# Performance work log

Hardware: AMD Instinct MI355X
Metric: run time of the kernel (lower is better)

Reference implementation:

```python
import jax, jax.numpy as jnp
from jax import lax
import numpy as np

GAMMA = 1.0
BIG = 1e10  # stands in for +inf; exp(-BIG/gamma) == 0 in fp32, safe under autodiff


def cosine_distance_matrix(x, y):
    # x: [B,N,d], y: [B,M,d] -> D: [B,N,M] = 1 - cos(x_i, y_j)
    xn = x / (jnp.linalg.norm(x, axis=-1, keepdims=True) + 1e-8)
    yn = y / (jnp.linalg.norm(y, axis=-1, keepdims=True) + 1e-8)
    return 1.0 - jnp.einsum('bnd,bmd->bnm', xn, yn)


def soft_dtw(D, gamma):
    # D: [B,N,M]. Returns R[:, N, M] of the soft-DTW DP:
    # R[i,j] = D[i-1,j-1] + softmin(R[i-1,j-1], R[i-1,j], R[i,j-1])
    B, N, M = D.shape
    # column j=0: R[:,0,0]=0, R[:,i,0]=inf for i>=1  -> shape [B, N+1]
    init_col = jnp.concatenate([jnp.zeros((B, 1), D.dtype),
                                jnp.full((B, N), BIG, D.dtype)], axis=1)

    def col_step(prev_col, d_col):
        # prev_col: R[:, 0:N+1, j-1]  [B, N+1];  d_col: D[:, :, j-1]  [B, N]
        def row_step(carry, inp):
            r_diag, r_up, d = inp  # each [B]: R[i-1,j-1], R[i-1,j]... (see below)
            stacked = jnp.stack([r_diag, carry, r_up], axis=0)  # [3,B]
            softmin = -gamma * jax.nn.logsumexp(-stacked / gamma, axis=0)
            r = d + softmin
            return r, r
        # per-row inputs along i=1..N: diag=prev_col[i-1], up-in-column=prev_col[i]
        inputs = (prev_col[:, :-1].T, prev_col[:, 1:].T, d_col.T)  # each [N,B]
        _, rows = lax.scan(row_step, jnp.full((B,), BIG, D.dtype), inputs)
        new_col = jnp.concatenate([jnp.full((B, 1), BIG, D.dtype), rows.T], axis=1)
        return new_col, None

    final_col, _ = lax.scan(col_step, init_col, jnp.transpose(D, (2, 0, 1)))
    return final_col[:, -1]  # R[:, N, M]


def setup_inputs() -> dict:
    key = jax.random.key(0)
    k1, k2 = jax.random.split(key)
    B, N, M, d = 16, 1024, 1024, 128
    x = jax.random.normal(k1, (B, N, d), dtype=jnp.float32)
    y = jax.random.normal(k2, (B, M, d), dtype=jnp.float32)
    return {"x": x, "y": y}


def reference(x, y):
    D = cosine_distance_matrix(x, y)
    return soft_dtw(D, GAMMA)  # [B]
```

## Files before the change

### kernel.cpp

```cpp
#include <hip/hip_runtime.h>
#include <hip/hip_fp16.h>

#define BATCH 16
#define NROW 1024
#define MCOL 1024
#define DFEAT 128

#define R_DP 16
#define C_DP 8
#define NCH (MCOL / C_DP)
#define PSTRIDE 194

#define L2E 1.4426950408889634f
#define LN2 0.6931471805599453f

typedef __attribute__((ext_vector_type(8))) short short8;
typedef __attribute__((ext_vector_type(4))) float f32x4;

__device__ inline unsigned short f2bf(float f) {
  unsigned u = __float_as_uint(f);
  return (unsigned short)((u + 0x7fff + ((u >> 16) & 1)) >> 16);
}

__global__ __launch_bounds__(256) void norm_kernel(
    const float* __restrict__ x, const float* __restrict__ y,
    unsigned short* __restrict__ xnb, unsigned short* __restrict__ ynb) {
  int row = blockIdx.x * 4 + (threadIdx.x >> 6);
  int lane = threadIdx.x & 63;
  const float* src;
  unsigned short* dst;
  if (row < BATCH * NROW) {
    src = x + (size_t)row * DFEAT;
    dst = xnb + (size_t)row * DFEAT;
  } else {
    int r2 = row - BATCH * NROW;
    src = y + (size_t)r2 * DFEAT;
    dst = ynb + (size_t)r2 * DFEAT;
  }
  float2 v = *(const float2*)(src + lane * 2);
  float s = v.x * v.x + v.y * v.y;
  #pragma unroll
  for (int o = 32; o > 0; o >>= 1) s += __shfl_xor(s, o, 64);
  float inv = 1.0f / (sqrtf(s) + 1e-8f);
  unsigned short b0 = f2bf(v.x * inv), b1 = f2bf(v.y * inv);
  *(unsigned*)(dst + lane * 2) = (unsigned)b0 | ((unsigned)b1 << 16);
}

__global__ __launch_bounds__(256) void dist_kernel(
    const unsigned short* __restrict__ xnb, const unsigned short* __restrict__ ynb,
    __half* __restrict__ Dphase) {
  __shared__ __align__(16) unsigned char xsb[128 * 256];
  __shared__ __align__(16) unsigned char ysb[128 * 256];

  int b = blockIdx.z, ti0 = blockIdx.y, tj0 = blockIdx.x;
  int I0 = ti0 * 128, J0 = tj0 * 128;
  int tid = threadIdx.x;

  const uint4* xsrc = (const uint4*)(xnb + (size_t)(b * NROW + I0) * DFEAT);
  const uint4* ysrc = (const uint4*)(ynb + (size_t)(b * MCOL + J0) * DFEAT);
  #pragma unroll
  for (int it = 0; it < 8; ++it) {
    int idx = tid + it * 256;
    int row = idx >> 4, cb = (idx & 15) * 16;
    int swz = row * 256 + (cb ^ ((row & 7) << 4));
    *(uint4*)&xsb[swz] = xsrc[idx];
    *(uint4*)&ysb[swz] = ysrc[idx];
  }
  __syncthreads();

  int wid = tid >> 6, lane = tid & 63;
  int wi = wid >> 1, wj = wid & 1;
  int lr = lane & 15, lk = lane >> 4;

  f32x4 acc[4][4] = {};
  #pragma unroll
  for (int ks = 0; ks < 4; ++ks) {
    int cb = ks * 64 + lk * 16;
    short8 af[4], bf[4];
    #pragma unroll
    for (int ti = 0; ti < 4; ++ti) {
      int row = wi * 64 + ti * 16 + lr;
      af[ti] = *(short8*)&xsb[row * 256 + (cb ^ ((row & 7) << 4))];
    }
    #pragma unroll
    for (int tj = 0; tj < 4; ++tj) {
      int row = wj * 64 + tj * 16 + lr;
      bf[tj] = *(short8*)&ysb[row * 256 + (cb ^ ((row & 7) << 4))];
    }
    #pragma unroll
    for (int ti = 0; ti < 4; ++ti)
      #pragma unroll
      for (int tj = 0; tj < 4; ++tj)
        acc[ti][tj] = __builtin_amdgcn_mfma_f32_16x16x32_bf16(
            af[ti], bf[tj], acc[ti][tj], 0, 0, 0);
  }

  #pragma unroll
  for (int ti = 0; ti < 4; ++ti) {
    int gi0 = I0 + wi * 64 + ti * 16;
    int l = gi0 >> 4;
    #pragma unroll
    for (int tj = 0; tj < 4; ++tj) {
      int gj = J0 + wj * 64 + tj * 16 + lr;
      int c = gj >> 3, k = gj & 7;
      int p = c + l;
      #pragma unroll
      for (int v = 0; v < 4; ++v) {
        int r = lk * 4 + v;
        float d = 1.0f - acc[ti][tj][v];
        size_t off = ((((size_t)b * PSTRIDE + p) * R_DP + r) * 64 + l) * C_DP + k;
        Dphase[off] = __float2half(exp2f(-d * L2E));
      }
    }
  }
}

__device__ __forceinline__ float shup(float x, bool edge) {
  int xi = __float_as_int(x);
  int sh = __builtin_amdgcn_update_dpp(xi, xi, 0x111, 0xF, 0xF, false);
  int bc = __builtin_amdgcn_update_dpp(xi, xi, 0x142, 0xF, 0xF, false);
  return __int_as_float(edge ? bc : sh);
}

#define MIXMUL_LO(A, h, s) \
  asm("v_fma_mix_f32 %0, %1, %2, %3 op_sel_hi:[1,0,0]" : "=v"(A) : "v"(h), "v"(s), "v"(fzero))
#define MIXMUL_HI(A, h, s) \
  asm("v_fma_mix_f32 %0, %1, %2, %3 op_sel:[1,0,0] op_sel_hi:[1,0,0]" : "=v"(A) : "v"(h), "v"(s), "v"(fzero))
#define MIXFMA_LO(lf, h, a) \
  asm("v_fma_mix_f32 %0, %1, %2, %3 op_sel_hi:[1,0,0]" : "=v"(lf) : "v"(h), "v"(lf), "v"(a))
#define MIXFMA_HI(lf, h, a) \
  asm("v_fma_mix_f32 %0, %1, %2, %3 op_sel:[1,0,0] op_sel_hi:[1,0,0]" : "=v"(lf) : "v"(h), "v"(lf), "v"(a))

template<bool GUARDED>
__device__ __forceinline__ void dtw_phase(int c, int t, bool edge,
    const uint4* L, float* carry, float (&B)[9], float& O, float fzero) {
  float U[9];
  #pragma unroll
  for (int k = 0; k < 9; ++k) U[k] = shup(B[k], edge);
  float Oin = shup(O, edge);
  if (t == 0) {
    #pragma unroll
    for (int k = 0; k < 9; ++k) U[k] = 0.0f;
    if (GUARDED && c == 0) U[0] = 1.0f;
    Oin = O;
  }
  bool act = GUARDED ? (c >= 0 && c < NCH) : true;
  if (act) {
    if (GUARDED && c == 0) O = Oin;
    float sc = exp2f((O - Oin) * L2E);
    #pragma unroll
    for (int k = 0; k < 9; ++k) U[k] *= sc;

    #pragma unroll
    for (int r = 0; r < R_DP; ++r) {
      uint4 d = L[r];
      unsigned dw[4] = {d.x, d.y, d.z, d.w};
      float S[8], A[8];
      #pragma unroll
      for (int k = 0; k < 8; ++k) S[k] = U[k] + U[k + 1];
      #pragma unroll
      for (int q = 0; q < 4; ++q) {
        MIXMUL_LO(A[2 * q],     dw[q], S[2 * q]);
        MIXMUL_HI(A[2 * q + 1], dw[q], S[2 * q + 1]);
      }
      float oldc = carry[r], lf = oldc;
      float V[8];
      #pragma unroll
      for (int q = 0; q < 4; ++q) {
        MIXFMA_LO(lf, dw[q], A[2 * q]);     V[2 * q] = lf;
        MIXFMA_HI(lf, dw[q], A[2 * q + 1]); V[2 * q + 1] = lf;
      }
      U[0] = oldc;
      #pragma unroll
      for (int k = 1; k <= 8; ++k) U[k] = V[k - 1];
      carry[r] = lf;
    }

    float rep = carry[R_DP - 1];
    int ex = (int)((__float_as_uint(rep) >> 23) & 0xFF) - 127;
    if ((ex < -20 || ex > 12) && ex < 128) {
      float s = __uint_as_float((unsigned)(127 - ex) << 23);
      #pragma unroll
      for (int r = 0; r < R_DP; ++r) carry[r] *= s;
      #pragma unroll
      for (int k = 0; k < 9; ++k) U[k] *= s;
      O -= (float)ex * LN2;
    }
    #pragma unroll
    for (int k = 0; k < 9; ++k) B[k] = U[k];
  }
}

#define GL(Lr, SB, OFF) \
  asm volatile("global_load_dwordx4 %0, %1, %2 offset:" OFF : "=v"(Lr) : "v"(voff), "s"(SB));

#define ISSUE16(L)                                               \
  GL(L[0],  s0, "0")    GL(L[1],  s0, "1024")                    \
  GL(L[2],  s0, "2048") GL(L[3],  s0, "3072")                    \
  GL(L[4],  s1, "0")    GL(L[5],  s1, "1024")                    \
  GL(L[6],  s1, "2048") GL(L[7],  s1, "3072")                    \
  GL(L[8],  s2, "0")    GL(L[9],  s2, "1024")                    \
  GL(L[10], s2, "2048") GL(L[11], s2, "3072")                    \
  GL(L[12], s3, "0")    GL(L[13], s3, "1024")                    \
  GL(L[14], s3, "2048") GL(L[15], s3, "3072")

#define ADV() { s0 += 16384; s1 += 16384; s2 += 16384; s3 += 16384; }

#define WAITC()                                       \
  asm volatile("s_waitcnt vmcnt(16)" ::: "memory");   \
  __builtin_amdgcn_sched_barrier(0);

#define STEP2(PP, G)                                                        \
  ADV(); ISSUE16(LB);                                                       \
  WAITC(); dtw_phase<G>((PP) - t, t, edge, LA, carry, B, O, fzero);         \
  ADV(); ISSUE16(LA);                                                       \
  WAITC(); dtw_phase<G>((PP) + 1 - t, t, edge, LB, carry, B, O, fzero);

__global__ __launch_bounds__(64, 1) void dtw_kernel(
    const __half* __restrict__ Dphase, float* __restrict__ out) {
  int b = blockIdx.x;
  int t = threadIdx.x;
  const bool edge = (t != 0) && ((t & 15) == 0);
  float fzero = 0.0f;
  int voff = t * 16;

  const char* g = (const char*)Dphase + (size_t)b * PSTRIDE * 16384;
  const char* s0 = g;
  const char* s1 = g + 4096;
  const char* s2 = g + 8192;
  const char* s3 = g + 12288;

  float carry[R_DP];
  #pragma unroll
  for (int r = 0; r < R_DP; ++r) carry[r] = 0.0f;
  float B[9] = {};
  float O = 0.0f;

  uint4 LA[R_DP], LB[R_DP];
  ISSUE16(LA);

  for (int p = 0; p < 64; p += 2)   { STEP2(p, true); }
  for (int p = 64; p < 128; p += 2) { STEP2(p, false); }
  for (int p = 128; p < 192; p += 2){ STEP2(p, true); }

  asm volatile("s_waitcnt vmcnt(0)" ::: "memory");

  if (t == 63) out[b] = O - logf(carry[R_DP - 1]);
}

extern "C" void kernel_launch(void* const* d_in, const int* in_sizes, int n_in,
                              void* d_out, int out_size, void* d_ws, size_t ws_size,
                              hipStream_t stream) {
  const float* x = (const float*)d_in[0];
  const float* y = (const float*)d_in[1];
  float* out = (float*)d_out;

  char* ws = (char*)d_ws;
  __half* Dphase = (__half*)ws;
  size_t dp_bytes = (size_t)BATCH * PSTRIDE * 16384;
  unsigned short* xnb = (unsigned short*)(ws + dp_bytes);
  unsigned short* ynb = xnb + (size_t)BATCH * NROW * DFEAT;

  norm_kernel<<<(2 * BATCH * NROW) / 4, 256, 0, stream>>>(x, y, xnb, ynb);
  dist_kernel<<<dim3(MCOL / 128, NROW / 128, BATCH), 256, 0, stream>>>(
      xnb, ynb, Dphase);
  dtw_kernel<<<BATCH, 64, 0, stream>>>(Dphase, out);
}
```

Measured before the change: 268.6 us.

## Split soft-DTW wavefront across four waves with shared-memory boundary handoff

The DP kernel moves from one 64-lane wave per batch to four waves per batch. Each wave owns a band of rows with 4 rows per lane instead of 16, and the waves pipeline along anti-diagonal phases, passing boundary values and offsets through LDS with a block barrier every phase. The distance matrix layout is rewritten into a triangular and parallelogram packed phase order so each wave can load its slice contiguously. This cuts serial work per phase so the sequential chain gets shorter, but it adds a barrier per step, twice as many phases, and more pipeline fill and drain.

```diff
diff --git a/kernel.cpp b/kernel.cpp
--- a/kernel.cpp
+++ b/kernel.cpp
@@ -6,10 +6,11 @@
 #define MCOL 1024
 #define DFEAT 128
 
-#define R_DP 16
+#define R_DP 4
 #define C_DP 8
 #define NCH (MCOL / C_DP)
-#define PSTRIDE 194
+#define NPHT 384
+#define BATCH_BYTES 2097152
 
 #define L2E 1.4426950408889634f
 #define LN2 0.6931471805599453f
@@ -20,6 +21,12 @@
 __device__ inline unsigned short f2bf(float f) {
   unsigned u = __float_as_uint(f);
   return (unsigned short)((u + 0x7fff + ((u >> 16) & 1)) >> 16);
+}
+
+__device__ __forceinline__ int pbase(int P) {
+  return (P < 128) ? 32 * P * (P + 1)
+       : (P < 256) ? 528384 + ((P - 128) << 13)
+                   : 1576960 + 32 * (16256 - (383 - P) * (384 - P));
 }
 
 __global__ __launch_bounds__(256) void norm_kernel(
@@ -48,7 +55,7 @@
 
 __global__ __launch_bounds__(256) void dist_kernel(
     const unsigned short* __restrict__ xnb, const unsigned short* __restrict__ ynb,
-    __half* __restrict__ Dphase) {
+    char* __restrict__ Dpar) {
   __shared__ __align__(16) unsigned char xsb[128 * 256];
   __shared__ __align__(16) unsigned char ysb[128 * 256];
 
@@ -95,32 +102,27 @@
             af[ti], bf[tj], acc[ti][tj], 0, 0, 0);
   }
 
+  char* Db = Dpar + (size_t)b * BATCH_BYTES;
   #pragma unroll
   for (int ti = 0; ti < 4; ++ti) {
-    int gi0 = I0 + wi * 64 + ti * 16;
-    int l = gi0 >> 4;
+    int gi0 = I0 + wi * 64 + ti * 16 + lk * 4;
+    int gl = gi0 >> 2;
     #pragma unroll
     for (int tj = 0; tj < 4; ++tj) {
       int gj = J0 + wj * 64 + tj * 16 + lr;
       int c = gj >> 3, k = gj & 7;
-      int p = c + l;
+      int P = c + gl;
+      int gmn = P > 127 ? P - 127 : 0;
+      char* slot = Db + pbase(P) + ((gl - gmn) << 6) + (k << 1);
       #pragma unroll
       for (int v = 0; v < 4; ++v) {
-        int r = lk * 4 + v;
         float d = 1.0f - acc[ti][tj][v];
-        size_t off = ((((size_t)b * PSTRIDE + p) * R_DP + r) * 64 + l) * C_DP + k;
-        Dphase[off] = __float2half(exp2f(-d * L2E));
+        *(__half*)(slot + v * 16) = __float2half(exp2f(-d * L2E));
       }
     }
   }
 }
 
-__device__ __forceinline__ float shup(float x, bool edge) {
-  int xi = __float_as_int(x);
-  int sh = __builtin_amdgcn_update_dpp(xi, xi, 0x111, 0xF, 0xF, false);
-  int bc = __builtin_amdgcn_update_dpp(xi, xi, 0x142, 0xF, 0xF, false);
-  return __int_as_float(edge ? bc : sh);
-}
 
 #define MIXMUL_LO(A, h, s) \
   asm("v_fma_mix_f32 %0, %1, %2, %3 op_sel_hi:[1,0,0]" : "=v"(A) : "v"(h), "v"(s), "v"(fzero))
@@ -131,22 +133,35 @@
 #define MIXFMA_HI(lf, h, a) \
   asm("v_fma_mix_f32 %0, %1, %2, %3 op_sel:[1,0,0] op_sel_hi:[1,0,0]" : "=v"(lf) : "v"(h), "v"(lf), "v"(a))
 
-template<bool GUARDED>
-__device__ __forceinline__ void dtw_phase(int c, int t, bool edge,
-    const uint4* L, float* carry, float (&B)[9], float& O, float fzero) {
+__device__ __forceinline__ float shup(float x, bool edge) {
+  int xi = __float_as_int(x);
+  int sh = __builtin_amdgcn_update_dpp(xi, xi, 0x111, 0xF, 0xF, false);
+  int bc = __builtin_amdgcn_update_dpp(xi, xi, 0x142, 0xF, 0xF, false);
+  return __int_as_float(edge ? bc : sh);
+}
+
+__device__ __forceinline__ void dtw_phase4(int cbase, int t, int w, bool edge,
+    const uint4* L, float* carry, float (&B)[9], float& O, float fzero,
+    const float* bndPrev) {
+  int c = cbase - t;
   float U[9];
   #pragma unroll
   for (int k = 0; k < 9; ++k) U[k] = shup(B[k], edge);
   float Oin = shup(O, edge);
   if (t == 0) {
-    #pragma unroll
-    for (int k = 0; k < 9; ++k) U[k] = 0.0f;
-    if (GUARDED && c == 0) U[0] = 1.0f;
-    Oin = O;
-  }
-  bool act = GUARDED ? (c >= 0 && c < NCH) : true;
-  if (act) {
-    if (GUARDED && c == 0) O = Oin;
+    if (w == 0) {
+      #pragma unroll
+      for (int k = 0; k < 9; ++k) U[k] = 0.0f;
+      U[0] = (c == 0) ? 1.0f : 0.0f;
+      Oin = O;
+    } else {
+      #pragma unroll
+      for (int k = 0; k < 9; ++k) U[k] = bndPrev[k];
+      Oin = bndPrev[9];
+    }
+  }
+  if ((unsigned)c < 128u) {
+    if (c == 0) O = Oin;
     float sc = exp2f((O - Oin) * L2E);
     #pragma unroll
     for (int k = 0; k < 9; ++k) U[k] *= sc;
@@ -191,61 +206,69 @@
   }
 }
 
-#define GL(Lr, SB, OFF) \
+#define GL4(Lr, SB, OFF) \
   asm volatile("global_load_dwordx4 %0, %1, %2 offset:" OFF : "=v"(Lr) : "v"(voff), "s"(SB));
-
-#define ISSUE16(L)                                               \
-  GL(L[0],  s0, "0")    GL(L[1],  s0, "1024")                    \
-  GL(L[2],  s0, "2048") GL(L[3],  s0, "3072")                    \
-  GL(L[4],  s1, "0")    GL(L[5],  s1, "1024")                    \
-  GL(L[6],  s1, "2048") GL(L[7],  s1, "3072")                    \
-  GL(L[8],  s2, "0")    GL(L[9],  s2, "1024")                    \
-  GL(L[10], s2, "2048") GL(L[11], s2, "3072")                    \
-  GL(L[12], s3, "0")    GL(L[13], s3, "1024")                    \
-  GL(L[14], s3, "2048") GL(L[15], s3, "3072")
-
-#define ADV() { s0 += 16384; s1 += 16384; s2 += 16384; s3 += 16384; }
-
-#define WAITC()                                       \
-  asm volatile("s_waitcnt vmcnt(16)" ::: "memory");   \
-  __builtin_amdgcn_sched_barrier(0);
-
-#define STEP2(PP, G)                                                        \
-  ADV(); ISSUE16(LB);                                                       \
-  WAITC(); dtw_phase<G>((PP) - t, t, edge, LA, carry, B, O, fzero);         \
-  ADV(); ISSUE16(LA);                                                       \
-  WAITC(); dtw_phase<G>((PP) + 1 - t, t, edge, LB, carry, B, O, fzero);
-
-__global__ __launch_bounds__(64, 1) void dtw_kernel(
-    const __half* __restrict__ Dphase, float* __restrict__ out) {
+#define ISSUE4(L, SB) \
+  GL4(L[0], SB, "0") GL4(L[1], SB, "16") GL4(L[2], SB, "32") GL4(L[3], SB, "48")
+
+#define STEP(P, CUR, NXT)                                                    \
+  {                                                                          \
+    int Pn = (P) + 1;                                                        \
+    int gmn = Pn > 127 ? Pn - 127 : 0;                                       \
+    const char* sb = gb + (pbase(Pn) + ((w64 - gmn) << 6));                  \
+    ISSUE4(NXT, sb)                                                          \
+    asm volatile("s_waitcnt vmcnt(4)" ::: "memory");                         \
+    __builtin_amdgcn_sched_barrier(0);                                       \
+    if ((unsigned)((P) - w64) < 191u) {                                      \
+      dtw_phase4((P) - w64, t, w, edge, CUR, carry, B, O, fzero,             \
+                 &bnd[(P) & 1][w > 0 ? w - 1 : 0][0]);                       \
+      if (t == 63) {                                                         \
+        float* bn = &bnd[((P) + 1) & 1][w][0];                               \
+        _Pragma("unroll")                                                    \
+        for (int k = 0; k < 9; ++k) bn[k] = B[k];                            \
+        bn[9] = O;                                                           \
+      }                                                                      \
+    }                                                                        \
+    asm volatile("s_waitcnt lgkmcnt(0)" ::: "memory");                       \
+    __builtin_amdgcn_s_barrier();                                            \
+    asm volatile("" ::: "memory");                                           \
+  }
+
+__global__ __launch_bounds__(256, 1) void dtw_kernel(
+    const char* __restrict__ Dpar, float* __restrict__ out) {
   int b = blockIdx.x;
-  int t = threadIdx.x;
+  int tid = threadIdx.x;
+  int w = __builtin_amdgcn_readfirstlane(tid >> 6);
+  int t = tid & 63;
+  int w64 = w << 6;
   const bool edge = (t != 0) && ((t & 15) == 0);
   float fzero = 0.0f;
-  int voff = t * 16;
-
-  const char* g = (const char*)Dphase + (size_t)b * PSTRIDE * 16384;
-  const char* s0 = g;
-  const char* s1 = g + 4096;
-  const char* s2 = g + 8192;
-  const char* s3 = g + 12288;
-
-  float carry[R_DP];
-  #pragma unroll
-  for (int r = 0; r < R_DP; ++r) carry[r] = 0.0f;
+  int voff = t << 6;
+
+  __shared__ float bnd[2][4][10];
+  if (tid < 80) ((float*)bnd)[tid] = 0.0f;
+  __syncthreads();
+
+  const char* gb = Dpar + (size_t)b * BATCH_BYTES;
+
+  float carry[R_DP] = {0.f, 0.f, 0.f, 0.f};
   float B[9] = {};
   float O = 0.0f;
 
   uint4 LA[R_DP], LB[R_DP];
-  ISSUE16(LA);
-
-  for (int p = 0; p < 64; p += 2)   { STEP2(p, true); }
-  for (int p = 64; p < 128; p += 2) { STEP2(p, false); }
-  for (int p = 128; p < 192; p += 2){ STEP2(p, true); }
+  {
+    const char* sb = gb + (w64 << 6);
+    ISSUE4(LA, sb)
+  }
+
+  for (int p = 0; p < NPHT; p += 2) {
+    STEP(p, LA, LB)
+    STEP(p + 1, LB, LA)
+  }
 
   asm volatile("s_waitcnt vmcnt(0)" ::: "memory");
 
-  if (t == 63) out[b] = O - logf(carry[R_DP - 1]);
+  if (tid == 255) out[b] = O - logf(carry[R_DP - 1]);
 }
 
 extern "C" void kernel_launch(void* const* d_in, const int* in_sizes, int n_in,
@@ -256,13 +279,13 @@
   float* out = (float*)d_out;
 
   char* ws = (char*)d_ws;
-  __half* Dphase = (__half*)ws;
-  size_t dp_bytes = (size_t)BATCH * PSTRIDE * 16384;
+  char* Dpar = ws;
+  size_t dp_bytes = (size_t)BATCH * BATCH_BYTES;
   unsigned short* xnb = (unsigned short*)(ws + dp_bytes);
   unsigned short* ynb = xnb + (size_t)BATCH * NROW * DFEAT;
 
   norm_kernel<<<(2 * BATCH * NROW) / 4, 256, 0, stream>>>(x, y, xnb, ynb);
   dist_kernel<<<dim3(MCOL / 128, NROW / 128, BATCH), 256, 0, stream>>>(
-      xnb, ynb, Dphase);
-  dtw_kernel<<<BATCH, 64, 0, stream>>>(Dphase, out);
-}
+      xnb, ynb, Dpar);
+  dtw_kernel<<<BATCH, 256, 0, stream>>>(Dpar, out);
+}
```

After: 292.5 us. 8.9% more time.

## Split DTW into producer/consumer waves with LDS ring buffer

Applied to the files above, without the earlier changes.

The DTW kernel now runs two waves per block. One wave issues the global loads of D-phase tiles and writes them into a 4-slot LDS ring. The other wave consumes the tiles from LDS and runs the wavefront recurrence, with the two synchronised through volatile shared counters and s_sleep spin-waits. This aims to take global-load latency and issue work off the serial compute wave, and it also skips loads for inactive lanes. In exchange it adds LDS round-trips, spin-wait overhead and relies on a hand-rolled memory ordering protocol.

```diff
diff --git a/kernel.cpp b/kernel.cpp
--- a/kernel.cpp
+++ b/kernel.cpp
@@ -9,6 +9,7 @@
 #define R_DP 16
 #define C_DP 8
 #define NCH (MCOL / C_DP)
+#define NPH_C 191
 #define PSTRIDE 194
 
 #define L2E 1.4426950408889634f
@@ -115,12 +116,6 @@
   }
 }
 
-__device__ __forceinline__ float shup(float x, bool edge) {
-  int xi = __float_as_int(x);
-  int sh = __builtin_amdgcn_update_dpp(xi, xi, 0x111, 0xF, 0xF, false);
-  int bc = __builtin_amdgcn_update_dpp(xi, xi, 0x142, 0xF, 0xF, false);
-  return __int_as_float(edge ? bc : sh);
-}
 
 #define MIXMUL_LO(A, h, s) \
   asm("v_fma_mix_f32 %0, %1, %2, %3 op_sel_hi:[1,0,0]" : "=v"(A) : "v"(h), "v"(s), "v"(fzero))
@@ -131,9 +126,16 @@
 #define MIXFMA_HI(lf, h, a) \
   asm("v_fma_mix_f32 %0, %1, %2, %3 op_sel:[1,0,0] op_sel_hi:[1,0,0]" : "=v"(lf) : "v"(h), "v"(lf), "v"(a))
 
+__device__ __forceinline__ float shup(float x, bool edge) {
+  int xi = __float_as_int(x);
+  int sh = __builtin_amdgcn_update_dpp(xi, xi, 0x111, 0xF, 0xF, false);
+  int bc = __builtin_amdgcn_update_dpp(xi, xi, 0x142, 0xF, 0xF, false);
+  return __int_as_float(edge ? bc : sh);
+}
+
 template<bool GUARDED>
-__device__ __forceinline__ void dtw_phase(int c, int t, bool edge,
-    const uint4* L, float* carry, float (&B)[9], float& O, float fzero) {
+__device__ __forceinline__ void dtw_phase_l(int c, int t, bool edge,
+    const uint4 (*slot)[64], float* carry, float (&B)[9], float& O, float fzero) {
   float U[9];
   #pragma unroll
   for (int k = 0; k < 9; ++k) U[k] = shup(B[k], edge);
@@ -144,7 +146,7 @@
     if (GUARDED && c == 0) U[0] = 1.0f;
     Oin = O;
   }
-  bool act = GUARDED ? (c >= 0 && c < NCH) : true;
+  bool act = GUARDED ? ((unsigned)c < 128u) : true;
   if (act) {
     if (GUARDED && c == 0) O = Oin;
     float sc = exp2f((O - Oin) * L2E);
@@ -153,7 +155,7 @@
 
     #pragma unroll
     for (int r = 0; r < R_DP; ++r) {
-      uint4 d = L[r];
+      uint4 d = slot[r][t];
       unsigned dw[4] = {d.x, d.y, d.z, d.w};
       float S[8], A[8];
       #pragma unroll
@@ -194,58 +196,102 @@
 #define GL(Lr, SB, OFF) \
   asm volatile("global_load_dwordx4 %0, %1, %2 offset:" OFF : "=v"(Lr) : "v"(voff), "s"(SB));
 
-#define ISSUE16(L)                                               \
-  GL(L[0],  s0, "0")    GL(L[1],  s0, "1024")                    \
-  GL(L[2],  s0, "2048") GL(L[3],  s0, "3072")                    \
-  GL(L[4],  s1, "0")    GL(L[5],  s1, "1024")                    \
-  GL(L[6],  s1, "2048") GL(L[7],  s1, "3072")                    \
-  GL(L[8],  s2, "0")    GL(L[9],  s2, "1024")                    \
-  GL(L[10], s2, "2048") GL(L[11], s2, "3072")                    \
-  GL(L[12], s3, "0")    GL(L[13], s3, "1024")                    \
-  GL(L[14], s3, "2048") GL(L[15], s3, "3072")
-
-#define ADV() { s0 += 16384; s1 += 16384; s2 += 16384; s3 += 16384; }
-
-#define WAITC()                                       \
-  asm volatile("s_waitcnt vmcnt(16)" ::: "memory");   \
-  __builtin_amdgcn_sched_barrier(0);
-
-#define STEP2(PP, G)                                                        \
-  ADV(); ISSUE16(LB);                                                       \
-  WAITC(); dtw_phase<G>((PP) - t, t, edge, LA, carry, B, O, fzero);         \
-  ADV(); ISSUE16(LA);                                                       \
-  WAITC(); dtw_phase<G>((PP) + 1 - t, t, edge, LB, carry, B, O, fzero);
-
-__global__ __launch_bounds__(64, 1) void dtw_kernel(
+#define ISSUE16(L, S0, S1, S2, S3)                               \
+  GL(L[0],  S0, "0")    GL(L[1],  S0, "1024")                    \
+  GL(L[2],  S0, "2048") GL(L[3],  S0, "3072")                    \
+  GL(L[4],  S1, "0")    GL(L[5],  S1, "1024")                    \
+  GL(L[6],  S1, "2048") GL(L[7],  S1, "3072")                    \
+  GL(L[8],  S2, "0")    GL(L[9],  S2, "1024")                    \
+  GL(L[10], S2, "2048") GL(L[11], S2, "3072")                    \
+  GL(L[12], S3, "0")    GL(L[13], S3, "1024")                    \
+  GL(L[14], S3, "2048") GL(L[15], S3, "3072")
+
+#define WRSLOT(SLOT, L)                                          \
+  _Pragma("unroll")                                              \
+  for (int r = 0; r < R_DP; ++r) ring[SLOT][r][t] = L[r];
+
+__global__ __launch_bounds__(128, 1) void dtw_kernel(
     const __half* __restrict__ Dphase, float* __restrict__ out) {
+  __shared__ __align__(16) uint4 ring[4][R_DP][64];
+  __shared__ volatile unsigned prodCnt, consCnt;
+
   int b = blockIdx.x;
-  int t = threadIdx.x;
-  const bool edge = (t != 0) && ((t & 15) == 0);
+  int tid = threadIdx.x;
+  int w = __builtin_amdgcn_readfirstlane(tid >> 6);
+  int t = tid & 63;
   float fzero = 0.0f;
   int voff = t * 16;
 
+  if (tid == 0) { prodCnt = 0; consCnt = 0; }
+  __syncthreads();
+
   const char* g = (const char*)Dphase + (size_t)b * PSTRIDE * 16384;
-  const char* s0 = g;
-  const char* s1 = g + 4096;
-  const char* s2 = g + 8192;
-  const char* s3 = g + 12288;
-
-  float carry[R_DP];
-  #pragma unroll
-  for (int r = 0; r < R_DP; ++r) carry[r] = 0.0f;
-  float B[9] = {};
-  float O = 0.0f;
-
-  uint4 LA[R_DP], LB[R_DP];
-  ISSUE16(LA);
-
-  for (int p = 0; p < 64; p += 2)   { STEP2(p, true); }
-  for (int p = 64; p < 128; p += 2) { STEP2(p, false); }
-  for (int p = 128; p < 192; p += 2){ STEP2(p, true); }
-
-  asm volatile("s_waitcnt vmcnt(0)" ::: "memory");
-
-  if (t == 63) out[b] = O - logf(carry[R_DP - 1]);
+
+  if (w == 1) {
+    uint4 A[R_DP], Bb[R_DP];
+    {
+      const char* s0 = g;
+      const char* s1 = g + 4096;
+      const char* s2 = g + 8192;
+      const char* s3 = g + 12288;
+      if ((unsigned)(0 - t) < 128u) { ISSUE16(A, s0, s1, s2, s3) }
+    }
+    for (int p = 0; p < 192; p += 2) {
+      {
+        int pn = (p + 1 > 190) ? 190 : p + 1;
+        const char* s0 = g + ((size_t)pn << 14);
+        const char* s1 = s0 + 4096;
+        const char* s2 = s0 + 8192;
+        const char* s3 = s0 + 12288;
+        if ((unsigned)(pn - t) < 128u) { ISSUE16(Bb, s0, s1, s2, s3) }
+        asm volatile("s_waitcnt vmcnt(16)" ::: "memory");
+        __builtin_amdgcn_sched_barrier(0);
+        while ((int)(p - (int)consCnt) >= 4) __builtin_amdgcn_s_sleep(8);
+        if ((unsigned)(p - t) < 128u) { WRSLOT(p & 3, A) }
+        asm volatile("s_waitcnt lgkmcnt(0)" ::: "memory");
+        if (t == 0) prodCnt = p + 1;
+      }
+      {
+        int pn = (p + 2 > 190) ? 190 : p + 2;
+        const char* s0 = g + ((size_t)pn << 14);
+        const char* s1 = s0 + 4096;
+        const char* s2 = s0 + 8192;
+        const char* s3 = s0 + 12288;
+        if ((unsigned)(pn - t) < 128u) { ISSUE16(A, s0, s1, s2, s3) }
+        asm volatile("s_waitcnt vmcnt(16)" ::: "memory");
+        __builtin_amdgcn_sched_barrier(0);
+        while ((int)((p + 1) - (int)consCnt) >= 4) __builtin_amdgcn_s_sleep(8);
+        if ((unsigned)((p + 1) - t) < 128u) { WRSLOT((p + 1) & 3, Bb) }
+        asm volatile("s_waitcnt lgkmcnt(0)" ::: "memory");
+        if (t == 0) prodCnt = p + 2;
+      }
+    }
+    asm volatile("s_waitcnt vmcnt(0)" ::: "memory");
+  } else {
+    const bool edge = (t != 0) && ((t & 15) == 0);
+    float carry[R_DP];
+    #pragma unroll
+    for (int r = 0; r < R_DP; ++r) carry[r] = 0.0f;
+    float B[9] = {};
+    float O = 0.0f;
+
+    #define CONSUME(P, G)                                                    \
+      {                                                                      \
+        while ((int)prodCnt < (P) + 1) __builtin_amdgcn_s_sleep(2);          \
+        asm volatile("s_waitcnt lgkmcnt(0)" ::: "memory");                   \
+        __builtin_amdgcn_sched_barrier(0);                                   \
+        dtw_phase_l<G>((P) - t, t, edge, ring[(P) & 3], carry, B, O, fzero); \
+        asm volatile("s_waitcnt lgkmcnt(0)" ::: "memory");                   \
+        if (t == 0) consCnt = (P) + 1;                                       \
+      }
+
+    for (int p = 0; p < 64; ++p)    CONSUME(p, true)
+    for (int p = 64; p < 128; ++p)  CONSUME(p, false)
+    for (int p = 128; p < 191; ++p) CONSUME(p, true)
+
+    if (t == 63) out[b] = O - logf(carry[R_DP - 1]);
+    #undef CONSUME
+  }
 }
 
 extern "C" void kernel_launch(void* const* d_in, const int* in_sizes, int n_in,
@@ -264,5 +310,5 @@
   norm_kernel<<<(2 * BATCH * NROW) / 4, 256, 0, stream>>>(x, y, xnb, ynb);
   dist_kernel<<<dim3(MCOL / 128, NROW / 128, BATCH), 256, 0, stream>>>(
       xnb, ynb, Dphase);
-  dtw_kernel<<<BATCH, 64, 0, stream>>>(Dphase, out);
-}
+  dtw_kernel<<<BATCH, 128, 0, stream>>>(Dphase, out);
+}
```

After: 286.2 us. +6.5%, slower.
